# Performance work log

Hardware: AMD Instinct MI355X
Metric: run time of the kernel (lower is better)

## Reference

```python
import jax, jax.numpy as jnp
import numpy as np

NUM_CARDS = 40
NUM_SUITS = 4
SIDE_SUIT_LEN = 9
NUM_ACTIONS = 2 * NUM_CARDS + 1  # 81 (use_signals=True)
NUM_TRICKS = 10


def setup_inputs() -> dict:
    key = jax.random.key(0)
    ks = jax.random.split(key, 8)
    B, A, D_in, D_q = 16384, 40, 4096, 256
    backbone_embed = jax.random.normal(ks[0], (B, D_in), dtype=jnp.float32)
    rank = jax.random.randint(ks[1], (B, A), -1, SIDE_SUIT_LEN)
    # guarantee at least one valid action per row (slot 0)
    rank = rank.at[:, 0].set(jnp.maximum(rank[:, 0], 0))
    suit = jax.random.randint(ks[2], (B, A), 0, NUM_SUITS + 1)  # suit==NUM_SUITS -> no-signal action
    valid_actions = jnp.stack([rank, suit], axis=-1)
    phase = jax.random.randint(ks[3], (B,), 0, 2)
    trick = jax.random.randint(ks[4], (B,), 0, NUM_TRICKS)
    # params
    Wq = jax.random.normal(ks[5], (D_in, D_q), dtype=jnp.float32) / np.sqrt(D_in).astype(np.float32)
    bq = jnp.zeros((D_q,), jnp.float32)
    key_table = jax.random.normal(ks[6], (NUM_ACTIONS, D_q), dtype=jnp.float32)
    ln_gamma = jnp.ones((D_q,), jnp.float32)
    ln_beta = jnp.zeros((D_q,), jnp.float32)
    # signal_prior == 'lin': p_signal = 2 / (num_tricks_left + 1)
    num_left = NUM_TRICKS - jnp.arange(NUM_TRICKS, dtype=jnp.float32)
    p_signal = 2.0 / (num_left + 1.0)
    return dict(backbone_embed=backbone_embed, valid_actions=valid_actions, phase=phase,
                trick=trick, Wq=Wq, bq=bq, key_table=key_table, ln_gamma=ln_gamma,
                ln_beta=ln_beta, p_signal=p_signal)


def reference(backbone_embed, valid_actions, phase, trick, Wq, bq, key_table, ln_gamma, ln_beta, p_signal):
    D_q = Wq.shape[1]
    rank = valid_actions[..., 0]          # (B, A)
    suit = valid_actions[..., 1]          # (B, A)
    aidx = phase[:, None] * NUM_CARDS + suit * SIDE_SUIT_LEN + rank
    aidx = jnp.where(rank == -1, -1, jnp.where(suit == NUM_SUITS, 2 * NUM_CARDS, aidx))
    # PaddedEmbed: shift by 1, row 0 is the zero padding row for idx == -1
    table = jnp.concatenate([jnp.zeros((1, D_q), key_table.dtype), key_table], axis=0)
    k = table[aidx + 1]                   # (B, A, D_q)
    # LayerNorm over last dim
    mu = k.mean(axis=-1, keepdims=True)
    var = k.var(axis=-1, keepdims=True)
    k = (k - mu) * jax.lax.rsqrt(var + 1e-5) * ln_gamma + ln_beta
    q = backbone_embed @ Wq + bq          # (B, D_q)
    attn = jnp.einsum('bq,baq->ba', q, k) / jnp.sqrt(jnp.float32(D_q))
    attn = jnp.where(rank == -1, -jnp.inf, attn)
    # no-signal bias on action 0 during signal phase
    n_valid = (rank != -1).sum(axis=-1).astype(jnp.float32)
    ps = p_signal[trick]
    w = jnp.log(jnp.maximum((1.0 - ps) / ps * (n_valid - 1.0), 1e-5))
    w = jnp.where(n_valid == 1.0, 0.0, w)
    attn = attn.at[:, 0].add(jnp.where(phase == 1, w, 0.0))
    return jax.nn.log_softmax(attn, axis=-1)
```

## Files before the change

### kernel.cpp

```cpp
#include <hip/hip_runtime.h>
#include <hip/hip_bf16.h>
#include <math.h>


typedef _Float16 half8_t __attribute__((ext_vector_type(8)));
typedef float    f32x4_t __attribute__((ext_vector_type(4)));

#define NUM_B 16384
#define D_IN  4096
#define D_Q   256
#define N_ACT 40
#define NPAD  96

__device__ __forceinline__ half8_t cvt8(const float4 a, const float4 b) {
  half8_t h;
  h[0] = (_Float16)a.x; h[1] = (_Float16)a.y; h[2] = (_Float16)a.z; h[3] = (_Float16)a.w;
  h[4] = (_Float16)b.x; h[5] = (_Float16)b.y; h[6] = (_Float16)b.z; h[7] = (_Float16)b.w;
  return h;
}
__device__ __forceinline__ void gl_lds16f(const float* g, float* l) {
  __builtin_amdgcn_global_load_lds(
      (const __attribute__((address_space(1))) void*)g,
      (__attribute__((address_space(3))) void*)l, 16, 0, 0);
}
__device__ __forceinline__ void gl_lds16h(const _Float16* g, _Float16* l) {
  __builtin_amdgcn_global_load_lds(
      (const __attribute__((address_space(1))) void*)g,
      (__attribute__((address_space(3))) void*)l, 16, 0, 0);
}

__global__ __launch_bounds__(256) void ln_table_k(const float* __restrict__ kt,
                                                  const float* __restrict__ gamma,
                                                  const float* __restrict__ beta,
                                                  const float* __restrict__ bq,
                                                  float* __restrict__ out,
                                                  float* __restrict__ bqk) {
  __shared__ float red[8];
  __shared__ float red2[4];
  const int t = threadIdx.x, r = blockIdx.x;
  float v = kt[r * 256 + t];
  float s = v, sq = v * v;
#pragma unroll
  for (int off = 1; off < 64; off <<= 1) {
    s  += __shfl_xor(s, off);
    sq += __shfl_xor(sq, off);
  }
  if ((t & 63) == 0) { red[t >> 6] = s; red[4 + (t >> 6)] = sq; }
  __syncthreads();
  s  = red[0] + red[1] + red[2] + red[3];
  sq = red[4] + red[5] + red[6] + red[7];
  const float mu  = s * (1.0f / 256.0f);
  const float var = sq * (1.0f / 256.0f) - mu * mu;
  const float inv = 1.0f / sqrtf(var + 1e-5f);
  const float o = (v - mu) * inv * gamma[t] + beta[t];
  out[r * 256 + t] = o;
  float p = o * bq[t];
#pragma unroll
  for (int off = 1; off < 64; off <<= 1) p += __shfl_xor(p, off);
  if ((t & 63) == 0) red2[t >> 6] = p;
  __syncthreads();
  if (t == 0) bqk[r] = red2[0] + red2[1] + red2[2] + red2[3];
}

__global__ __launch_bounds__(256) void wk_gemm_k(const float* __restrict__ Wq,
                                                 const float* __restrict__ tbl,
                                                 _Float16* __restrict__ Bf) {
  const int lane = threadIdx.x & 63, w = threadIdx.x >> 6;
  const int wm = w >> 1, wn = w & 1;
  const int m0 = blockIdx.x * 64 + wm * 32;
  const int n0 = wn * 48;
  const int fr = lane & 15, fg = lane >> 4;
  f32x4_t acc[2][3] = {};
  for (int k0 = 0; k0 < 256; k0 += 32) {
    half8_t af[2], bf[3];
#pragma unroll
    for (int i = 0; i < 2; ++i) {
      const float* p = Wq + (size_t)(m0 + i * 16 + fr) * D_Q + k0 + fg * 8;
      af[i] = cvt8(*(const float4*)p, *(const float4*)(p + 4));
    }
#pragma unroll
    for (int j = 0; j < 3; ++j) {
      const int n = n0 + j * 16 + fr;
      if (n < 81) {
        const float* p = tbl + (size_t)n * D_Q + k0 + fg * 8;
        bf[j] = cvt8(*(const float4*)p, *(const float4*)(p + 4));
      } else {
        bf[j] = (half8_t)(_Float16)0.0f;
      }
    }
#pragma unroll
    for (int i = 0; i < 2; ++i)
#pragma unroll
      for (int j = 0; j < 3; ++j)
        acc[i][j] = __builtin_amdgcn_mfma_f32_16x16x32_f16(af[i], bf[j], acc[i][j], 0, 0, 0);
  }
#pragma unroll
  for (int i = 0; i < 2; ++i)
#pragma unroll
    for (int j = 0; j < 3; ++j)
#pragma unroll
      for (int r = 0; r < 4; ++r) {
        const int k = m0 + i * 16 + fg * 4 + r;
        const int n = n0 + j * 16 + fr;
        Bf[(((size_t)(k >> 5) * 6 + (n >> 4)) * 64 +
            (((k >> 3) & 3) * 16 + (n & 15))) * 8 + (k & 7)] =
            (_Float16)acc[i][j][r];
      }
}

__global__ __launch_bounds__(512) void gemm_part_k(const float* __restrict__ A,
                                                   const _Float16* __restrict__ Bf,
                                                   float* __restrict__ part) {
  __shared__ __align__(16) char smem[57344];
  float*    Afs = (float*)smem;
  _Float16* Bls = (_Float16*)(smem + 32768);

  const int t = threadIdx.x, lane = t & 63, w = t >> 6;
  const int fr = lane & 15, fg = lane >> 4;
  const int ks = blockIdx.y;
  const size_t row0 = (size_t)blockIdx.x * 64;
  const int k0 = ks * 2048;

#define STAGE(T, P)                                                           \
  do {                                                                        \
    if (w < 4) {                                                              \
      float* abase = Afs + (P)*4096;                                          \
      _Pragma("unroll") for (int q_ = 0; q_ < 4; ++q_) {                      \
        const int id_ = w * 4 + q_;                                           \
        const int r_ = id_ * 4 + (lane >> 4);                                 \
        gl_lds16f(A + (size_t)(row0 + r_) * D_IN + k0 + (T)*64 +              \
                      (((lane & 15) ^ (r_ & 7)) << 2),                        \
                  abase + id_ * 256);                                         \
      }                                                                       \
    } else {                                                                  \
      _Float16* bbase = Bls + (P)*6144;                                       \
      _Pragma("unroll") for (int q_ = 0; q_ < 3; ++q_) {                      \
        const int ib_ = (w - 4) * 3 + q_;                                     \
        gl_lds16h(Bf + ((size_t)(ks * 64 + (T)*2 + (ib_ / 6)) * 6 +           \
                        (ib_ % 6)) * 512 + lane * 8,                          \
                  bbase + ib_ * 512);                                         \
      }                                                                       \
    }                                                                         \
  } while (0)

  const int wm = w >> 1, wn = w & 1;
  int aoff[2][2];
#pragma unroll
  for (int c = 0; c < 2; ++c)
#pragma unroll
    for (int h = 0; h < 2; ++h) {
      const int R = wm * 16 + fr;
      aoff[c][h] = R * 64 + (((c * 8 + fg * 2 + h) ^ (R & 7)) << 2);
    }
  int boff[2][3];
#pragma unroll
  for (int c = 0; c < 2; ++c)
#pragma unroll
    for (int j = 0; j < 3; ++j)
      boff[c][j] = c * 3072 + (wn * 3 + j) * 512 + lane * 8;

  f32x4_t acc[3] = {};

  STAGE(0, 0);
  for (int kt = 0; kt < 32; ++kt) {
    if (kt < 31) STAGE(kt + 1, (kt + 1) & 1);
    __builtin_amdgcn_sched_barrier(0);
    if (kt < 31) {
      if (w < 4) asm volatile("s_waitcnt vmcnt(4)" ::: "memory");
      else       asm volatile("s_waitcnt vmcnt(3)" ::: "memory");
    } else {
      asm volatile("s_waitcnt vmcnt(0)" ::: "memory");
    }
    __builtin_amdgcn_s_barrier();
    __builtin_amdgcn_sched_barrier(0);

    const float*    Ap = Afs + (kt & 1) * 4096;
    const _Float16* Bp = Bls + (kt & 1) * 6144;
#pragma unroll
    for (int c = 0; c < 2; ++c) {
      half8_t bfv[3];
#pragma unroll
      for (int j = 0; j < 3; ++j) bfv[j] = *(const half8_t*)(Bp + boff[c][j]);
      const float4 x0 = *(const float4*)(Ap + aoff[c][0]);
      const float4 x1 = *(const float4*)(Ap + aoff[c][1]);
      const half8_t af = cvt8(x0, x1);
#pragma unroll
      for (int j = 0; j < 3; ++j)
        acc[j] = __builtin_amdgcn_mfma_f32_16x16x32_f16(af, bfv[j], acc[j], 0, 0, 0);
    }
    asm volatile("s_waitcnt lgkmcnt(0)" ::: "memory");
    __builtin_amdgcn_s_barrier();
    __builtin_amdgcn_sched_barrier(0);
  }
#undef STAGE

  float* pb = part + ((size_t)ks * NUM_B + row0) * NPAD;
#pragma unroll
  for (int j = 0; j < 3; ++j) {
    const int col = wn * 48 + j * 16 + fr;
#pragma unroll
    for (int r = 0; r < 4; ++r)
      pb[(size_t)(wm * 16 + fg * 4 + r) * NPAD + col] = acc[j][r];
  }
}

__global__ __launch_bounds__(256) void softmax_k(const float* __restrict__ part,
                                                 const float* __restrict__ bqk,
                                                 const int* __restrict__ va,
                                                 const int* __restrict__ phase,
                                                 const int* __restrict__ trick,
                                                 const float* __restrict__ psig,
                                                 float* __restrict__ out) {
  const int t = threadIdx.x;
  const int lane = t & 63, w = t >> 6;
  const int b = blockIdx.x * 4 + w;

  float sx = 0.f, sy = 0.f;
  if (lane < 48) {
#pragma unroll
    for (int ks = 0; ks < 2; ++ks) {
      const float2 v = *(const float2*)&part[((size_t)ks * NUM_B + b) * NPAD + lane * 2];
      sx += v.x; sy += v.y;
    }
  }

  int rank = -1, suit = 0;
  if (lane < N_ACT) {
    rank = va[((size_t)b * N_ACT + lane) * 2];
    suit = va[((size_t)b * N_ACT + lane) * 2 + 1];
  }
  const int ph = phase[b];
  const bool valid = (rank >= 0);
  const int aidx = valid ? (suit == 4 ? 80 : ph * 40 + suit * 9 + rank) : -1;
  const int nvalid = __popcll(__ballot(valid));

  const int srcl = valid ? (aidx >> 1) : 0;
  const float v0 = __shfl(sx, srcl);
  const float v1 = __shfl(sy, srcl);

  float attn_l = -INFINITY;
  if (valid) attn_l = (((aidx & 1) ? v1 : v0) + bqk[aidx]) * 0.0625f;

  if (ph == 1 && lane == 0) {
    const float ps = psig[trick[b]];
    const float nv = (float)nvalid;
    const float wv = (nv == 1.0f) ? 0.0f
                                  : logf(fmaxf((1.0f - ps) / ps * (nv - 1.0f), 1e-5f));
    attn_l += wv;
  }

  float m = attn_l;
#pragma unroll
  for (int off = 1; off < 64; off <<= 1) m = fmaxf(m, __shfl_xor(m, off));
  const float e = expf(attn_l - m);
  float ssum = e;
#pragma unroll
  for (int off = 1; off < 64; off <<= 1) ssum += __shfl_xor(ssum, off);
  const float o = attn_l - m - logf(ssum);
  if (lane < N_ACT) out[(size_t)b * N_ACT + lane] = valid ? o : -3.0e38f;
}

extern "C" void kernel_launch(void* const* d_in, const int* in_sizes, int n_in,
                              void* d_out, int out_size, void* d_ws, size_t ws_size,
                              hipStream_t stream) {
  const float* backbone = (const float*)d_in[0];
  const int*   va       = (const int*)d_in[1];
  const int*   phase    = (const int*)d_in[2];
  const int*   trick    = (const int*)d_in[3];
  const float* Wq       = (const float*)d_in[4];
  const float* bq       = (const float*)d_in[5];
  const float* keytab   = (const float*)d_in[6];
  const float* gamma    = (const float*)d_in[7];
  const float* beta     = (const float*)d_in[8];
  const float* psig     = (const float*)d_in[9];
  float* out = (float*)d_out;

  char* ws = (char*)d_ws;
  _Float16* Bf   = (_Float16*)ws;
  float* tableLN = (float*)(ws + (1u << 20));
  float* bqk     = (float*)(ws + (1u << 20) + (128u << 10));
  float* part    = (float*)(ws + (2u << 20));

  ln_table_k<<<dim3(81), 256, 0, stream>>>(keytab, gamma, beta, bq, tableLN, bqk);
  wk_gemm_k<<<dim3(64), 256, 0, stream>>>(Wq, tableLN, Bf);
  gemm_part_k<<<dim3(NUM_B / 64, 2), 512, 0, stream>>>(backbone, Bf, part);
  softmax_k<<<dim3(NUM_B / 4), 256, 0, stream>>>(part, bqk, va, phase, trick,
                                                 psig, out);
}
```

Measured before the change: 83.93 us.

## Retile split-K GEMM to 128-row blocks with 4-way K split

The main GEMM block tile grows from 64 to 128 rows, and the K split grows from 2 to 4 ways, so the grid stays at 512 blocks. The K step per stage drops from 64 to 32, and every wave now issues loads instead of splitting into A-loader and B-loader waves. Each B fragment is reused across two A row tiles, which cuts B traffic to shared memory and the LDS footprint. In exchange, the softmax kernel must sum 4 partial buffers instead of 2, which doubles the partial-result write and read traffic.

After: 92.00 us. +9.6%, slower.

```diff
diff --git a/kernel.cpp b/kernel.cpp
--- a/kernel.cpp
+++ b/kernel.cpp
@@ -111,34 +111,29 @@
 __global__ __launch_bounds__(512) void gemm_part_k(const float* __restrict__ A,
                                                    const _Float16* __restrict__ Bf,
                                                    float* __restrict__ part) {
-  __shared__ __align__(16) char smem[57344];
+  __shared__ __align__(16) char smem[45056];
   float*    Afs = (float*)smem;
   _Float16* Bls = (_Float16*)(smem + 32768);
 
   const int t = threadIdx.x, lane = t & 63, w = t >> 6;
   const int fr = lane & 15, fg = lane >> 4;
   const int ks = blockIdx.y;
-  const size_t row0 = (size_t)blockIdx.x * 64;
-  const int k0 = ks * 2048;
+  const size_t row0 = (size_t)blockIdx.x * 128;
+  const int k0 = ks * 1024;
 
 #define STAGE(T, P)                                                           \
   do {                                                                        \
-    if (w < 4) {                                                              \
-      float* abase = Afs + (P)*4096;                                          \
-      _Pragma("unroll") for (int q_ = 0; q_ < 4; ++q_) {                      \
-        const int id_ = w * 4 + q_;                                           \
-        const int r_ = id_ * 4 + (lane >> 4);                                 \
-        gl_lds16f(A + (size_t)(row0 + r_) * D_IN + k0 + (T)*64 +              \
-                      (((lane & 15) ^ (r_ & 7)) << 2),                        \
-                  abase + id_ * 256);                                         \
-      }                                                                       \
-    } else {                                                                  \
-      _Float16* bbase = Bls + (P)*6144;                                       \
-      _Pragma("unroll") for (int q_ = 0; q_ < 3; ++q_) {                      \
-        const int ib_ = (w - 4) * 3 + q_;                                     \
-        gl_lds16h(Bf + ((size_t)(ks * 64 + (T)*2 + (ib_ / 6)) * 6 +           \
-                        (ib_ % 6)) * 512 + lane * 8,                          \
-                  bbase + ib_ * 512);                                         \
+    _Pragma("unroll") for (int q_ = 0; q_ < 3; ++q_) {                        \
+      const int id_ = w * 3 + q_;                                             \
+      if (id_ < 16) {                                                         \
+        const int r_ = id_ * 8 + (lane >> 3);                                 \
+        gl_lds16f(A + (size_t)(row0 + r_) * D_IN + k0 + (T)*32 +              \
+                      (((lane & 7) ^ (r_ & 7)) << 2),                         \
+                  Afs + (P)*4096 + id_ * 256);                                \
+      } else if (id_ < 22) {                                                  \
+        const int jg_ = id_ - 16;                                             \
+        gl_lds16h(Bf + ((size_t)(ks * 32 + (T)) * 6 + jg_) * 512 + lane * 8,  \
+                  Bls + (P)*3072 + jg_ * 512);                                \
       }                                                                       \
     }                                                                         \
   } while (0)
@@ -146,28 +141,25 @@
   const int wm = w >> 1, wn = w & 1;
   int aoff[2][2];
 #pragma unroll
-  for (int c = 0; c < 2; ++c)
+  for (int i = 0; i < 2; ++i)
 #pragma unroll
     for (int h = 0; h < 2; ++h) {
-      const int R = wm * 16 + fr;
-      aoff[c][h] = R * 64 + (((c * 8 + fg * 2 + h) ^ (R & 7)) << 2);
-    }
-  int boff[2][3];
-#pragma unroll
-  for (int c = 0; c < 2; ++c)
-#pragma unroll
-    for (int j = 0; j < 3; ++j)
-      boff[c][j] = c * 3072 + (wn * 3 + j) * 512 + lane * 8;
-
-  f32x4_t acc[3] = {};
+      const int R = wm * 32 + i * 16 + fr;
+      aoff[i][h] = R * 32 + (((fg * 2 + h) ^ (R & 7)) << 2);
+    }
+  int boff[3];
+#pragma unroll
+  for (int j = 0; j < 3; ++j) boff[j] = (wn * 3 + j) * 512 + lane * 8;
+
+  f32x4_t acc[2][3] = {};
 
   STAGE(0, 0);
   for (int kt = 0; kt < 32; ++kt) {
     if (kt < 31) STAGE(kt + 1, (kt + 1) & 1);
     __builtin_amdgcn_sched_barrier(0);
     if (kt < 31) {
-      if (w < 4) asm volatile("s_waitcnt vmcnt(4)" ::: "memory");
-      else       asm volatile("s_waitcnt vmcnt(3)" ::: "memory");
+      if (w < 7) asm volatile("s_waitcnt vmcnt(3)" ::: "memory");
+      else       asm volatile("s_waitcnt vmcnt(1)" ::: "memory");
     } else {
       asm volatile("s_waitcnt vmcnt(0)" ::: "memory");
     }
@@ -175,18 +167,18 @@
     __builtin_amdgcn_sched_barrier(0);
 
     const float*    Ap = Afs + (kt & 1) * 4096;
-    const _Float16* Bp = Bls + (kt & 1) * 6144;
-#pragma unroll
-    for (int c = 0; c < 2; ++c) {
-      half8_t bfv[3];
-#pragma unroll
-      for (int j = 0; j < 3; ++j) bfv[j] = *(const half8_t*)(Bp + boff[c][j]);
-      const float4 x0 = *(const float4*)(Ap + aoff[c][0]);
-      const float4 x1 = *(const float4*)(Ap + aoff[c][1]);
+    const _Float16* Bp = Bls + (kt & 1) * 3072;
+    half8_t bfv[3];
+#pragma unroll
+    for (int j = 0; j < 3; ++j) bfv[j] = *(const half8_t*)(Bp + boff[j]);
+#pragma unroll
+    for (int i = 0; i < 2; ++i) {
+      const float4 x0 = *(const float4*)(Ap + aoff[i][0]);
+      const float4 x1 = *(const float4*)(Ap + aoff[i][1]);
       const half8_t af = cvt8(x0, x1);
 #pragma unroll
       for (int j = 0; j < 3; ++j)
-        acc[j] = __builtin_amdgcn_mfma_f32_16x16x32_f16(af, bfv[j], acc[j], 0, 0, 0);
+        acc[i][j] = __builtin_amdgcn_mfma_f32_16x16x32_f16(af, bfv[j], acc[i][j], 0, 0, 0);
     }
     asm volatile("s_waitcnt lgkmcnt(0)" ::: "memory");
     __builtin_amdgcn_s_barrier();
@@ -196,12 +188,14 @@
 
   float* pb = part + ((size_t)ks * NUM_B + row0) * NPAD;
 #pragma unroll
-  for (int j = 0; j < 3; ++j) {
-    const int col = wn * 48 + j * 16 + fr;
-#pragma unroll
-    for (int r = 0; r < 4; ++r)
-      pb[(size_t)(wm * 16 + fg * 4 + r) * NPAD + col] = acc[j][r];
-  }
+  for (int i = 0; i < 2; ++i)
+#pragma unroll
+    for (int j = 0; j < 3; ++j) {
+      const int col = wn * 48 + j * 16 + fr;
+#pragma unroll
+      for (int r = 0; r < 4; ++r)
+        pb[(size_t)(wm * 32 + i * 16 + fg * 4 + r) * NPAD + col] = acc[i][j][r];
+    }
 }
 
 __global__ __launch_bounds__(256) void softmax_k(const float* __restrict__ part,
@@ -218,7 +212,7 @@
   float sx = 0.f, sy = 0.f;
   if (lane < 48) {
 #pragma unroll
-    for (int ks = 0; ks < 2; ++ks) {
+    for (int ks = 0; ks < 4; ++ks) {
       const float2 v = *(const float2*)&part[((size_t)ks * NUM_B + b) * NPAD + lane * 2];
       sx += v.x; sy += v.y;
     }
@@ -283,7 +277,7 @@
 
   ln_table_k<<<dim3(81), 256, 0, stream>>>(keytab, gamma, beta, bq, tableLN, bqk);
   wk_gemm_k<<<dim3(64), 256, 0, stream>>>(Wq, tableLN, Bf);
-  gemm_part_k<<<dim3(NUM_B / 64, 2), 512, 0, stream>>>(backbone, Bf, part);
+  gemm_part_k<<<dim3(NUM_B / 128, 4), 512, 0, stream>>>(backbone, Bf, part);
   softmax_k<<<dim3(NUM_B / 4), 256, 0, stream>>>(part, bqk, va, phase, trick,
                                                  psig, out);
 }
```
